# Optimization experiments

Hardware: AMD Instinct MI355X
Metric: run time of the kernel (lower is better)

The kernel has to match this reference:

```python
import jax, jax.numpy as jnp
import numpy as np

B, D, N, MSRC, H = 4, 256, 2048, 2048, 4
DIM = D // H  # per-head dim = 64
EPS = 1e-3


def _conv1x1(W, b, z):
    # 1x1 Conv1d == per-position linear: W [out,in], z [B,in,N]
    return jnp.einsum('oc,bcn->bon', W, z) + b[None, :, None]


def setup_inputs() -> dict:
    key = jax.random.key(0)
    ks = jax.random.split(key, 20)
    s = 0.05
    x = jax.random.normal(ks[0], (B, D, N), dtype=jnp.float32)
    source = jax.random.normal(ks[1], (B, D, MSRC), dtype=jnp.float32)
    mask = (jax.random.uniform(ks[2], (B, N, MSRC)) > 0.3).astype(jnp.float32)
    Wq = jax.random.normal(ks[3], (D, D), jnp.float32) * s
    bq = jax.random.normal(ks[4], (D,), jnp.float32) * s
    Wk = jax.random.normal(ks[5], (D, D), jnp.float32) * s
    bk = jax.random.normal(ks[6], (D,), jnp.float32) * s
    Wv = jax.random.normal(ks[7], (D, D), jnp.float32) * s
    bv = jax.random.normal(ks[8], (D,), jnp.float32) * s
    Wm = jax.random.normal(ks[9], (D, D), jnp.float32) * s
    bm = jax.random.normal(ks[10], (D,), jnp.float32) * s
    W1 = jax.random.normal(ks[11], (2 * D, 2 * D), jnp.float32) * s
    b1 = jax.random.normal(ks[12], (2 * D,), jnp.float32) * s
    gamma = jnp.ones((2 * D,), jnp.float32)
    beta = jnp.zeros((2 * D,), jnp.float32)
    rmean = jax.random.normal(ks[13], (2 * D,), jnp.float32) * 0.1
    rvar = jax.random.uniform(ks[14], (2 * D,), jnp.float32) + 0.5
    W2 = jax.random.normal(ks[15], (D, 2 * D), jnp.float32) * s
    b2 = jnp.zeros((D,), jnp.float32)  # nn.init.constant_(mlp[-1].bias, 0.0)
    return dict(x=x, source=source, mask=mask, Wq=Wq, bq=bq, Wk=Wk, bk=bk,
                Wv=Wv, bv=bv, Wm=Wm, bm=bm, W1=W1, b1=b1, gamma=gamma,
                beta=beta, rmean=rmean, rvar=rvar, W2=W2, b2=b2)


def reference(x, source, mask, Wq, bq, Wk, bk, Wv, bv, Wm, bm,
              W1, b1, gamma, beta, rmean, rvar, W2, b2):
    b = x.shape[0]
    # channel dim split as (dim, heads) per torch .view(B, dim, H, -1)
    q = _conv1x1(Wq, bq, x).reshape(b, DIM, H, -1)        # [B,d,H,N]
    k = _conv1x1(Wk, bk, source).reshape(b, DIM, H, -1)   # [B,d,H,M]
    v = _conv1x1(Wv, bv, source).reshape(b, DIM, H, -1)   # [B,d,H,M]
    scores = jnp.einsum('bdhn,bdhm->bhnm', q, k) / (DIM ** 0.5)
    neg = -jnp.finfo(scores.dtype).max
    scores = jnp.where(mask[:, None, :, :] > 0, scores, neg)
    prob = jax.nn.softmax(scores, axis=-1)                # [B,H,N,M]
    msg = jnp.einsum('bhnm,bdhm->bdhn', prob, v).reshape(b, D, -1)
    message = _conv1x1(Wm, bm, msg)                       # [B,D,N]
    y = jnp.concatenate([x, message], axis=1)             # [B,2D,N]
    h = _conv1x1(W1, b1, y)
    # BatchNorm1d (eval mode, eps=1e-3)
    h = (h - rmean[None, :, None]) * jax.lax.rsqrt(rvar + EPS)[None, :, None]
    h = h * gamma[None, :, None] + beta[None, :, None]
    h = jax.nn.relu(h)
    return _conv1x1(W2, b2, h)                            # [B,D,N]
```

## Files before the change

### kernel.cpp

```cpp
#include <hip/hip_runtime.h>

constexpr int Bb = 4;
constexpr int Dd = 256;
constexpr int Nn = 2048;
constexpr int Mm = 2048;
constexpr int Hh = 4;
constexpr int D2 = 512;
constexpr int NT = Bb * Nn;

#define FMAXV 3.402823466e38f

typedef _Float16 half8 __attribute__((ext_vector_type(8)));
typedef _Float16 half4v __attribute__((ext_vector_type(4)));
typedef float f32x4 __attribute__((ext_vector_type(4)));

typedef const __attribute__((address_space(1))) void* gas_p;
typedef __attribute__((address_space(3))) void* las_p;

__device__ __forceinline__ void gload16(const void* g, void* l) {
    __builtin_amdgcn_global_load_lds((gas_p)g, (las_p)l, 16, 0, 0);
}

__global__ __launch_bounds__(256)
void prep_all_kernel(const float* __restrict__ Wq, const float* __restrict__ bq,
                     const float* __restrict__ Wk, const float* __restrict__ bk,
                     const float* __restrict__ Wv, const float* __restrict__ bv,
                     const float* __restrict__ Wm,
                     const float* __restrict__ W1, const float* __restrict__ b1,
                     const float* __restrict__ gamma, const float* __restrict__ beta,
                     const float* __restrict__ rmean, const float* __restrict__ rvar,
                     const float* __restrict__ W2, const float* __restrict__ mask,
                     const float* __restrict__ x, const float* __restrict__ source,
                     _Float16* __restrict__ Wqp, float* __restrict__ bqp,
                     _Float16* __restrict__ Wkvp, float* __restrict__ bkvp,
                     _Float16* __restrict__ Wmp,
                     _Float16* __restrict__ W1p, float* __restrict__ b1f,
                     _Float16* __restrict__ W2p,
                     unsigned long long* __restrict__ bmask,
                     _Float16* __restrict__ Yp, _Float16* __restrict__ Sp) {
    const int r = blockIdx.x, t = threadIdx.x;
    if (r < 256) {
        const int h = r >> 6, d = r & 63, so = d * Hh + h;
        Wqp[r * 256 + t] = (_Float16)Wq[so * 256 + t];
        if (t == 0) bqp[r] = bq[so];
    } else if (r < 768) {
        const int rr = r - 256, part = rr >> 8, o = rr & 255;
        const int h = o >> 6, d = o & 63, so = d * Hh + h;
        const float* Ws = part ? Wv : Wk;
        const float* bs = part ? bv : bk;
        Wkvp[rr * 256 + t] = (_Float16)Ws[so * 256 + t];
        if (t == 0) bkvp[rr] = bs[so];
    } else if (r < 1024) {
        const int o = r - 768;
        const int h = t >> 6, d = t & 63, sk = d * Hh + h;
        Wmp[o * 256 + t] = (_Float16)Wm[o * 256 + sk];
    } else if (r < 1536) {
        const int o = r - 1024;
        const float s = gamma[o] * rsqrtf(rvar[o] + 1e-3f);
        W1p[o * 512 + t]       = (_Float16)(W1[o * 512 + t] * s);
        W1p[o * 512 + t + 256] = (_Float16)(W1[o * 512 + t + 256] * s);
        if (t == 0) b1f[o] = (b1[o] - rmean[o]) * s + beta[o];
    } else if (r < 1792) {
        const int o = r - 1536;
        W2p[o * 512 + t]       = (_Float16)W2[o * 512 + t];
        W2p[o * 512 + t + 256] = (_Float16)W2[o * 512 + t + 256];
    } else if (r < 3840) {
        const int id = r - 1792;
        const int w = t >> 6, lane = t & 63;
        const int row = id * 4 + w;
        const float* mrow = mask + (size_t)row * Mm;
        unsigned long long* brow = bmask + (size_t)row * (Mm / 64);
        #pragma unroll 4
        for (int word = 0; word < Mm / 64; ++word) {
            const float v = mrow[word * 64 + lane];
            const unsigned long long bits = __ballot(v > 0.f);
            if (lane == 0) brow[word] = bits;
        }
    } else {
        __shared__ _Float16 Ts[64][72];
        const int px = r - 3840;
        const int n0 = (px & 31) * 64, c0 = ((px >> 5) & 3) * 64;
        const int z = px >> 7, b = z >> 1, which = z & 1;
        const float* src = which ? source : x;
        _Float16* dst = which ? Sp : Yp;
        const int stride = which ? 256 : 512;
        const int cl = t >> 2, np = (t & 3) * 16;
        const float* sp = src + ((size_t)b * Dd + c0 + cl) * Nn + n0 + np;
        #pragma unroll
        for (int i = 0; i < 4; ++i) {
            float4 v = *(const float4*)(sp + i * 4);
            Ts[np + i * 4 + 0][cl] = (_Float16)v.x;
            Ts[np + i * 4 + 1][cl] = (_Float16)v.y;
            Ts[np + i * 4 + 2][cl] = (_Float16)v.z;
            Ts[np + i * 4 + 3][cl] = (_Float16)v.w;
        }
        __syncthreads();
        const int nl = t >> 2, cp = (t & 3) * 16;
        half8 a0 = *(const half8*)&Ts[nl][cp];
        half8 a1 = *(const half8*)&Ts[nl][cp + 8];
        _Float16* dp = dst + ((size_t)b * Nn + n0 + nl) * stride + c0 + cp;
        *(half8*)dp = a0;
        *(half8*)(dp + 8) = a1;
    }
}

__global__ __launch_bounds__(256)
void gemm4w_kernel(const _Float16* __restrict__ A, const _Float16* __restrict__ A2,
                   const _Float16* __restrict__ W, const float* __restrict__ bias,
                   _Float16* __restrict__ dst0, _Float16* __restrict__ dst1,
                   _Float16* __restrict__ dst2, float* __restrict__ dstF,
                   int K, int sA, int sOut, int modeSel, int relu, float oscale) {
    __shared__ __align__(16) _Float16 As[2 * 128 * 64];
    __shared__ __align__(16) _Float16 Bs[2 * 64 * 64];

    const int t = threadIdx.x;
    const int w = t >> 6, lane = t & 63, quad = lane >> 4, l16 = lane & 15;
    const int n0 = blockIdx.x * 128;
    const int og0 = blockIdx.y * 64;

    int mode = 0, oloc0 = og0;
    const _Float16* Ab = A;
    int sAl = sA;
    _Float16* d0 = dst0;
    float osc = oscale;
    if (modeSel == 3) {
        const int part = blockIdx.y >> 2;
        if (part == 1)      { Ab = A2; sAl = 256; d0 = dst1; oloc0 = og0 - 256; osc = 1.0f; }
        else if (part == 2) { Ab = A2; sAl = 256; mode = 1; oloc0 = og0 - 512; osc = 1.0f; }
    } else if (modeSel == 2) {
        mode = 2;
    }

    const int srow = t >> 3, sslot = t & 7;
    const int schunk = sslot ^ (srow & 7);

    f32x4 acc[2][4] = {};
    const int nk = K / 64;
    int buf = 0;

    {
        #pragma unroll
        for (int c = 0; c < 4; ++c)
            gload16(Ab + (size_t)(n0 + c * 32 + srow) * sAl + schunk * 8,
                    As + c * 2048 + t * 8);
        #pragma unroll
        for (int c = 0; c < 2; ++c)
            gload16(W + (size_t)(og0 + c * 32 + srow) * K + schunk * 8,
                    Bs + c * 2048 + t * 8);
        __asm__ volatile("s_waitcnt vmcnt(0)" ::: "memory");
        __syncthreads();
    }

    #pragma unroll 1
    for (int kt = 0; kt < nk; ++kt) {
        if (kt + 1 < nk) {
            const int k0 = (kt + 1) * 64, nb = buf ^ 1;
            #pragma unroll
            for (int c = 0; c < 4; ++c)
                gload16(Ab + (size_t)(n0 + c * 32 + srow) * sAl + k0 + schunk * 8,
                        As + nb * 8192 + c * 2048 + t * 8);
            #pragma unroll
            for (int c = 0; c < 2; ++c)
                gload16(W + (size_t)(og0 + c * 32 + srow) * K + k0 + schunk * 8,
                        Bs + nb * 4096 + c * 2048 + t * 8);
        }
        #pragma unroll
        for (int ks = 0; ks < 2; ++ks) {
            const int csw = ((ks * 4 + quad) ^ (l16 & 7)) * 8;
            half8 af[2], bf[4];
            #pragma unroll
            for (int i = 0; i < 2; ++i)
                af[i] = *(const half8*)&As[buf * 8192 + (w * 32 + i * 16 + l16) * 64 + csw];
            #pragma unroll
            for (int j = 0; j < 4; ++j)
                bf[j] = *(const half8*)&Bs[buf * 4096 + (j * 16 + l16) * 64 + csw];
            #pragma unroll
            for (int i = 0; i < 2; ++i)
                #pragma unroll
                for (int j = 0; j < 4; ++j)
                    acc[i][j] = __builtin_amdgcn_mfma_f32_16x16x32_f16(af[i], bf[j], acc[i][j], 0, 0, 0);
        }
        if (kt + 1 < nk) {
            __asm__ volatile("s_waitcnt vmcnt(0)" ::: "memory");
            __syncthreads();
            buf ^= 1;
        }
    }

    float bcol[4];
    #pragma unroll
    for (int j = 0; j < 4; ++j) bcol[j] = bias[og0 + j * 16 + l16];

    if (mode == 0) {
        _Float16* Escr = As + w * 2048;
        #pragma unroll
        for (int i = 0; i < 2; ++i) {
            #pragma unroll
            for (int j = 0; j < 4; ++j)
                #pragma unroll
                for (int reg = 0; reg < 4; ++reg) {
                    float v = (acc[i][j][reg] + bcol[j]) * osc;
                    if (relu) v = fmaxf(v, 0.f);
                    Escr[(quad * 4 + reg) * 72 + j * 16 + l16] = (_Float16)v;
                }
            __asm__ volatile("s_waitcnt lgkmcnt(0)" ::: "memory");
            const int row = lane & 15, oseg = (lane >> 4) * 16;
            half8 e0 = *(const half8*)&Escr[row * 72 + oseg];
            half8 e1 = *(const half8*)&Escr[row * 72 + oseg + 8];
            _Float16* dp = d0 + (size_t)(n0 + w * 32 + i * 16 + row) * sOut + oloc0 + oseg;
            *(half8*)dp = e0;
            *(half8*)(dp + 8) = e1;
            __asm__ volatile("s_waitcnt lgkmcnt(0)" ::: "memory");
        }
    } else if (mode == 1) {
        #pragma unroll
        for (int i = 0; i < 2; ++i)
            #pragma unroll
            for (int j = 0; j < 4; ++j) {
                const int c = j * 16 + l16;
                const int mloc = w * 32 + i * 16 + quad * 4;
                const int sw = l16 * 8;
                half4v pv;
                #pragma unroll
                for (int reg = 0; reg < 4; ++reg)
                    pv[reg] = (_Float16)(acc[i][j][reg] + bcol[j]);
                *(half4v*)&As[c * 128 + (mloc ^ sw)] = pv;
            }
        __syncthreads();
        const int n0m = n0 & 2047, bidx = n0 >> 11;
        #pragma unroll
        for (int r = 0; r < 2; ++r) {
            const int c = (t >> 3) + r * 32;
            const int mch = (t & 7) * 16;
            const int sw = (c & 15) * 8;
            half8 v0 = *(const half8*)&As[c * 128 + (mch ^ sw)];
            half8 v1 = *(const half8*)&As[c * 128 + ((mch + 8) ^ sw)];
            _Float16* dp = dst2 + ((size_t)bidx * 256 + oloc0 + c) * (size_t)Mm + n0m + mch;
            *(half8*)dp = v0;
            *(half8*)(dp + 8) = v1;
        }
    } else {
        __syncthreads();
        float* scr = (float*)As;
        #pragma unroll
        for (int i = 0; i < 2; ++i)
            #pragma unroll
            for (int j = 0; j < 4; ++j) {
                const int c = j * 16 + l16;
                const int mloc = w * 32 + i * 16 + quad * 4;
                const int sw = (c & 7) * 4;
                f32x4 v;
                #pragma unroll
                for (int reg = 0; reg < 4; ++reg) v[reg] = acc[i][j][reg] + bcol[j];
                *(f32x4*)&scr[c * 128 + (mloc ^ sw)] = v;
            }
        __syncthreads();
        const int n0m = n0 & 2047, bidx = n0 >> 11;
        #pragma unroll
        for (int r = 0; r < 2; ++r) {
            const int c = (t >> 3) + r * 32;
            const int mch = (t & 7) * 16;
            const int sw = (c & 7) * 4;
            float* dp = dstF + ((size_t)bidx * 256 + og0 + c) * (size_t)Nn + n0m + mch;
            #pragma unroll
            for (int k = 0; k < 4; ++k)
                *(f32x4*)(dp + k * 4) = *(const f32x4*)&scr[c * 128 + ((mch + k * 4) ^ sw)];
        }
    }
}

__global__ __launch_bounds__(256)
void attn_mfma_kernel(const _Float16* __restrict__ Qp, const _Float16* __restrict__ Kp,
                      const _Float16* __restrict__ Vt,
                      const unsigned int* __restrict__ bmask,
                      _Float16* __restrict__ Oa, _Float16* __restrict__ Ob,
                      float* __restrict__ La, float* __restrict__ Lb) {
    __shared__ __align__(16) _Float16 Ks[64][72];
    __shared__ __align__(16) _Float16 Vs[64][72];
    __shared__ __align__(16) _Float16 Ps[4][16][72];

    const int id = blockIdx.x;
    const int xcd = id & 7, loc = id >> 3;
    const int bh = xcd * 2 + (loc >> 6);
    const int sub = loc & 63;
    const int mhalf = sub & 1;
    const int n0 = (sub >> 1) * 64;
    const int b = bh >> 2, h = bh & 3;

    const int t = threadIdx.x;
    const int w = t >> 6, lane = t & 63, quad = lane >> 4, l16 = lane & 15;

    const _Float16* qp = Qp + ((size_t)b * Nn + n0 + w * 16 + l16) * 256 + h * 64 + quad * 8;
    const half8 qa0 = *(const half8*)(qp);
    const half8 qa1 = *(const half8*)(qp + 32);

    const _Float16* Kstg = Kp + (size_t)b * Nn * 256 + h * 64;
    const _Float16* Vstg = Vt + ((size_t)b * 256 + h * 64) * (size_t)Mm;
    const int sr = t >> 2, sc = (t & 3) * 16;

    const unsigned int* bmBase = bmask + ((size_t)b * Nn + n0 + w * 16 + quad * 4) * (Mm / 32);

    _Float16* Od = mhalf ? Ob : Oa;
    float* Ld = mhalf ? Lb : La;
    const int mbeg = mhalf * (Mm / 2);

    float lo[4] = {0.f, 0.f, 0.f, 0.f};
    f32x4 O[4] = {};

    half8 sk0, sk1, sv0, sv1;
    auto stage_load = [&](int m0) {
        const _Float16* ks = Kstg + (size_t)(m0 + sr) * 256 + sc;
        sk0 = *(const half8*)(ks);
        sk1 = *(const half8*)(ks + 8);
        const _Float16* vs = Vstg + (size_t)sr * Mm + m0 + sc;
        sv0 = *(const half8*)(vs);
        sv1 = *(const half8*)(vs + 8);
    };
    auto stage_write = [&]() {
        *(half8*)&Ks[sr][sc]     = sk0;
        *(half8*)&Ks[sr][sc + 8] = sk1;
        *(half8*)&Vs[sr][sc]     = sv0;
        *(half8*)&Vs[sr][sc + 8] = sv1;
    };

    stage_load(mbeg);
    stage_write();
    __syncthreads();

    #pragma unroll 1
    for (int it = 0; it < (Mm / 2) / 64; ++it) {
        const int m0 = mbeg + it * 64;
        if (it < (Mm / 2) / 64 - 1) stage_load(m0 + 64);

        uint2 bmv[4];
        #pragma unroll
        for (int reg = 0; reg < 4; ++reg)
            bmv[reg] = *(const uint2*)(bmBase + (size_t)reg * (Mm / 32) + (m0 >> 5));

        f32x4 S[4];
        #pragma unroll
        for (int mt = 0; mt < 4; ++mt) {
            half8 k0 = *(const half8*)&Ks[mt * 16 + l16][quad * 8];
            half8 k1 = *(const half8*)&Ks[mt * 16 + l16][32 + quad * 8];
            f32x4 z = {0.f, 0.f, 0.f, 0.f};
            z = __builtin_amdgcn_mfma_f32_16x16x32_f16(qa0, k0, z, 0, 0, 0);
            z = __builtin_amdgcn_mfma_f32_16x16x32_f16(qa1, k1, z, 0, 0, 0);
            S[mt] = z;
        }

        float p[4][4];
        #pragma unroll
        for (int reg = 0; reg < 4; ++reg) {
            const unsigned losh = bmv[reg].x >> l16;
            const unsigned hish = bmv[reg].y >> l16;
            p[0][reg] = (losh & 1u)         ? __expf(S[0][reg]) : 0.f;
            p[1][reg] = ((losh >> 16) & 1u) ? __expf(S[1][reg]) : 0.f;
            p[2][reg] = (hish & 1u)         ? __expf(S[2][reg]) : 0.f;
            p[3][reg] = ((hish >> 16) & 1u) ? __expf(S[3][reg]) : 0.f;
        }
        #pragma unroll
        for (int reg = 0; reg < 4; ++reg)
            lo[reg] += (p[0][reg] + p[1][reg]) + (p[2][reg] + p[3][reg]);

        #pragma unroll
        for (int mt = 0; mt < 4; ++mt)
            #pragma unroll
            for (int reg = 0; reg < 4; ++reg)
                Ps[w][quad * 4 + reg][mt * 16 + l16] = (_Float16)p[mt][reg];
        __asm__ volatile("s_waitcnt lgkmcnt(0)" ::: "memory");
        half8 pa0 = *(const half8*)&Ps[w][l16][quad * 8];
        half8 pa1 = *(const half8*)&Ps[w][l16][32 + quad * 8];

        #pragma unroll
        for (int dt = 0; dt < 4; ++dt) {
            half8 v0 = *(const half8*)&Vs[dt * 16 + l16][quad * 8];
            half8 v1 = *(const half8*)&Vs[dt * 16 + l16][32 + quad * 8];
            O[dt] = __builtin_amdgcn_mfma_f32_16x16x32_f16(pa0, v0, O[dt], 0, 0, 0);
            O[dt] = __builtin_amdgcn_mfma_f32_16x16x32_f16(pa1, v1, O[dt], 0, 0, 0);
        }

        if (it < (Mm / 2) / 64 - 1) {
            __syncthreads();
            stage_write();
            __syncthreads();
        }
    }

    #pragma unroll
    for (int reg = 0; reg < 4; ++reg) {
        float s = lo[reg];
        s += __shfl_xor(s, 1);
        s += __shfl_xor(s, 2);
        s += __shfl_xor(s, 4);
        s += __shfl_xor(s, 8);
        lo[reg] = s;
    }

    _Float16* op = Od + ((size_t)b * Nn + n0 + w * 16 + quad * 4) * 256 + h * 64 + l16;
    #pragma unroll
    for (int reg = 0; reg < 4; ++reg)
        #pragma unroll
        for (int dt = 0; dt < 4; ++dt)
            op[(size_t)reg * 256 + dt * 16] = (_Float16)(O[dt][reg] * 0.0625f);
    if (l16 == 0) {
        #pragma unroll
        for (int reg = 0; reg < 4; ++reg)
            Ld[((size_t)b * Nn + n0 + w * 16 + quad * 4 + reg) * 4 + h] = lo[reg] * 0.0625f;
    }
}

__global__ __launch_bounds__(256)
void gemm_msg_kernel(const _Float16* __restrict__ Oa, const _Float16* __restrict__ Ob,
                     const float* __restrict__ La, const float* __restrict__ Lb,
                     const _Float16* __restrict__ W, const float* __restrict__ bias,
                     _Float16* __restrict__ dst) {
    __shared__ __align__(16) _Float16 As[2 * 128 * 64];
    __shared__ __align__(16) _Float16 Bs[2 * 64 * 64];

    const int t = threadIdx.x;
    const int w = t >> 6, lane = t & 63, quad = lane >> 4, l16 = lane & 15;
    const int n0 = blockIdx.x * 128;
    const int og0 = blockIdx.y * 64;
    const int srow = t >> 3, sslot = t & 7;
    const int schunk = sslot ^ (srow & 7);
    constexpr int K = 256;

    f32x4 acc[2][4] = {};

    half8 oa[4], ob[4];
    float inv[4];

    auto loadA = [&](int k0) {
        const int h = k0 >> 6;
        #pragma unroll
        for (int c = 0; c < 4; ++c) {
            const size_t row = (size_t)(n0 + c * 32 + srow);
            oa[c] = *(const half8*)(Oa + row * 256 + k0 + schunk * 8);
            ob[c] = *(const half8*)(Ob + row * 256 + k0 + schunk * 8);
            inv[c] = 1.0f / (La[row * 4 + h] + Lb[row * 4 + h]);
        }
    };
    auto writeA = [&](int nb) {
        #pragma unroll
        for (int c = 0; c < 4; ++c) {
            half8 m;
            #pragma unroll
            for (int k = 0; k < 8; ++k)
                m[k] = (_Float16)(((float)oa[c][k] + (float)ob[c][k]) * inv[c]);
            *(half8*)&As[nb * 8192 + c * 2048 + t * 8] = m;
        }
    };
    auto loadB = [&](int k0, int nb) {
        #pragma unroll
        for (int c = 0; c < 2; ++c)
            gload16(W + (size_t)(og0 + c * 32 + srow) * K + k0 + schunk * 8,
                    Bs + nb * 4096 + c * 2048 + t * 8);
    };

    loadA(0);
    loadB(0, 0);
    writeA(0);
    __asm__ volatile("s_waitcnt vmcnt(0)" ::: "memory");
    __syncthreads();

    int buf = 0;
    #pragma unroll 1
    for (int kt = 0; kt < 4; ++kt) {
        if (kt < 3) {
            loadA((kt + 1) * 64);
            loadB((kt + 1) * 64, buf ^ 1);
        }
        #pragma unroll
        for (int ks = 0; ks < 2; ++ks) {
            const int csw = ((ks * 4 + quad) ^ (l16 & 7)) * 8;
            half8 af[2], bf[4];
            #pragma unroll
            for (int i = 0; i < 2; ++i)
                af[i] = *(const half8*)&As[buf * 8192 + (w * 32 + i * 16 + l16) * 64 + csw];
            #pragma unroll
            for (int j = 0; j < 4; ++j)
                bf[j] = *(const half8*)&Bs[buf * 4096 + (j * 16 + l16) * 64 + csw];
            #pragma unroll
            for (int i = 0; i < 2; ++i)
                #pragma unroll
                for (int j = 0; j < 4; ++j)
                    acc[i][j] = __builtin_amdgcn_mfma_f32_16x16x32_f16(af[i], bf[j], acc[i][j], 0, 0, 0);
        }
        if (kt < 3) {
            writeA(buf ^ 1);
            __asm__ volatile("s_waitcnt vmcnt(0)" ::: "memory");
            __syncthreads();
            buf ^= 1;
        }
    }

    float bcol[4];
    #pragma unroll
    for (int j = 0; j < 4; ++j) bcol[j] = bias[og0 + j * 16 + l16];

    _Float16* Escr = As + w * 2048;
    #pragma unroll
    for (int i = 0; i < 2; ++i) {
        #pragma unroll
        for (int j = 0; j < 4; ++j)
            #pragma unroll
            for (int reg = 0; reg < 4; ++reg)
                Escr[(quad * 4 + reg) * 72 + j * 16 + l16] =
                    (_Float16)(acc[i][j][reg] + bcol[j]);
        __asm__ volatile("s_waitcnt lgkmcnt(0)" ::: "memory");
        const int row = lane & 15, oseg = (lane >> 4) * 16;
        half8 e0 = *(const half8*)&Escr[row * 72 + oseg];
        half8 e1 = *(const half8*)&Escr[row * 72 + oseg + 8];
        _Float16* dp = dst + (size_t)(n0 + w * 32 + i * 16 + row) * 512 + og0 + oseg;
        *(half8*)dp = e0;
        *(half8*)(dp + 8) = e1;
        __asm__ volatile("s_waitcnt lgkmcnt(0)" ::: "memory");
    }
}

extern "C" void kernel_launch(void* const* d_in, const int* in_sizes, int n_in,
                              void* d_out, int out_size, void* d_ws, size_t ws_size,
                              hipStream_t stream) {
    const float* x      = (const float*)d_in[0];
    const float* source = (const float*)d_in[1];
    const float* mask   = (const float*)d_in[2];
    const float* Wq = (const float*)d_in[3];
    const float* bq = (const float*)d_in[4];
    const float* Wk = (const float*)d_in[5];
    const float* bk = (const float*)d_in[6];
    const float* Wv = (const float*)d_in[7];
    const float* bv = (const float*)d_in[8];
    const float* Wm = (const float*)d_in[9];
    const float* bm = (const float*)d_in[10];
    const float* W1 = (const float*)d_in[11];
    const float* b1 = (const float*)d_in[12];
    const float* gamma = (const float*)d_in[13];
    const float* beta  = (const float*)d_in[14];
    const float* rmean = (const float*)d_in[15];
    const float* rvar  = (const float*)d_in[16];
    const float* W2 = (const float*)d_in[17];
    const float* b2 = (const float*)d_in[18];
    float* outp = (float*)d_out;

    char* wsb = (char*)d_ws;
    _Float16* Yp   = (_Float16*)wsb;
    _Float16* Sp   = (_Float16*)(wsb + (8u << 20));
    _Float16* Qp   = (_Float16*)(wsb + (12u << 20));
    _Float16* Kp   = (_Float16*)(wsb + (16u << 20));
    _Float16* Vt   = (_Float16*)(wsb + (20u << 20));
    _Float16* Oa   = (_Float16*)(wsb + (24u << 20));
    _Float16* Hp   = (_Float16*)(wsb + (28u << 20));
    unsigned long long* bmask = (unsigned long long*)(wsb + (28u << 20));
    _Float16* Ob = (_Float16*)(wsb + (30u << 20));
    float* La = (float*)(wsb + (34u << 20));
    float* Lb = (float*)(wsb + (34u << 20) + (128u << 10));
    char* wp = wsb + (36u << 20);
    _Float16* Wqp  = (_Float16*)wp;            wp += 256 * 256 * 2;
    _Float16* Wkvp = (_Float16*)wp;            wp += 512 * 256 * 2;
    _Float16* Wmp  = (_Float16*)wp;            wp += 256 * 256 * 2;
    _Float16* W1p  = (_Float16*)wp;            wp += 512 * 512 * 2;
    _Float16* W2p  = (_Float16*)wp;            wp += 256 * 512 * 2;
    float* bqp  = (float*)wp;                  wp += 256 * 4;
    float* bkvp = (float*)wp;                  wp += 512 * 4;
    float* b1f  = (float*)wp;                  wp += 512 * 4;

    prep_all_kernel<<<4864, 256, 0, stream>>>(
        Wq, bq, Wk, bk, Wv, bv, Wm, W1, b1, gamma, beta, rmean, rvar, W2, mask,
        x, source, Wqp, bqp, Wkvp, bkvp, Wmp, W1p, b1f, W2p, bmask, Yp, Sp);

    gemm4w_kernel<<<dim3(NT / 128, 12), 256, 0, stream>>>(
        Yp, Sp, Wqp, bqp, Qp, Kp, Vt, nullptr, 256, 512, 256, 3, 0, 0.125f);

    attn_mfma_kernel<<<1024, 256, 0, stream>>>(Qp, Kp, Vt,
                                               (const unsigned int*)bmask,
                                               Oa, Ob, La, Lb);

    gemm_msg_kernel<<<dim3(NT / 128, 4), 256, 0, stream>>>(
        Oa, Ob, La, Lb, Wmp, bm, Yp + 256);

    gemm4w_kernel<<<dim3(NT / 128, 8), 256, 0, stream>>>(
        Yp, nullptr, W1p, b1f, Hp, nullptr, nullptr, nullptr, 512, 512, 512, 0, 1, 1.0f);
    gemm4w_kernel<<<dim3(NT / 128, 4), 256, 0, stream>>>(
        Hp, nullptr, W2p, b2, nullptr, nullptr, nullptr, outp, 512, 512, 0, 2, 0, 1.0f);
}
```

Before: 233.3 us.

## Split attention KV range into four partitions and XOR-swizzle K/V LDS tiles

The attention kernel now splits the key range into four quarters instead of two, doubling the grid to 2048 blocks. Each block writes partial outputs and row sums to one of four buffers, and the message GEMM merges all four. The Sp buffer and the final output buffer are reused as scratch for the extra partials. K/V shared tiles drop their padding and use an XOR swizzle on 16-byte chunks to avoid bank conflicts. The change adds more partial-result traffic and merge work, and depends on the reused buffers being dead at this point.

```diff
diff --git a/kernel.cpp b/kernel.cpp
--- a/kernel.cpp
+++ b/kernel.cpp
@@ -274,17 +274,19 @@
                       const _Float16* __restrict__ Vt,
                       const unsigned int* __restrict__ bmask,
                       _Float16* __restrict__ Oa, _Float16* __restrict__ Ob,
-                      float* __restrict__ La, float* __restrict__ Lb) {
-    __shared__ __align__(16) _Float16 Ks[64][72];
-    __shared__ __align__(16) _Float16 Vs[64][72];
+                      _Float16* __restrict__ Oc, _Float16* __restrict__ Od,
+                      float* __restrict__ La, float* __restrict__ Lb,
+                      float* __restrict__ Lc, float* __restrict__ Ld) {
+    __shared__ __align__(16) _Float16 Ks[64][64];
+    __shared__ __align__(16) _Float16 Vs[64][64];
     __shared__ __align__(16) _Float16 Ps[4][16][72];
 
     const int id = blockIdx.x;
     const int xcd = id & 7, loc = id >> 3;
-    const int bh = xcd * 2 + (loc >> 6);
-    const int sub = loc & 63;
-    const int mhalf = sub & 1;
-    const int n0 = (sub >> 1) * 64;
+    const int bh = xcd * 2 + (loc >> 7);
+    const int sub = loc & 127;
+    const int mquart = sub & 3;
+    const int n0 = (sub >> 2) * 64;
     const int b = bh >> 2, h = bh & 3;
 
     const int t = threadIdx.x;
@@ -296,13 +298,16 @@
 
     const _Float16* Kstg = Kp + (size_t)b * Nn * 256 + h * 64;
     const _Float16* Vstg = Vt + ((size_t)b * 256 + h * 64) * (size_t)Mm;
-    const int sr = t >> 2, sc = (t & 3) * 16;
+    const int sr = t >> 2;
+    const int sc = (t & 3) * 16;
+    const int ss0 = ((t & 3) * 2) ^ (sr & 7);
+    const int ss1 = ((t & 3) * 2 + 1) ^ (sr & 7);
 
     const unsigned int* bmBase = bmask + ((size_t)b * Nn + n0 + w * 16 + quad * 4) * (Mm / 32);
 
-    _Float16* Od = mhalf ? Ob : Oa;
-    float* Ld = mhalf ? Lb : La;
-    const int mbeg = mhalf * (Mm / 2);
+    _Float16* Odst = mquart == 0 ? Oa : mquart == 1 ? Ob : mquart == 2 ? Oc : Od;
+    float*    Ldst = mquart == 0 ? La : mquart == 1 ? Lb : mquart == 2 ? Lc : Ld;
+    const int mbeg = mquart * (Mm / 4);
 
     float lo[4] = {0.f, 0.f, 0.f, 0.f};
     f32x4 O[4] = {};
@@ -317,10 +322,10 @@
         sv1 = *(const half8*)(vs + 8);
     };
     auto stage_write = [&]() {
-        *(half8*)&Ks[sr][sc]     = sk0;
-        *(half8*)&Ks[sr][sc + 8] = sk1;
-        *(half8*)&Vs[sr][sc]     = sv0;
-        *(half8*)&Vs[sr][sc + 8] = sv1;
+        *(half8*)&Ks[sr][ss0 * 8] = sk0;
+        *(half8*)&Ks[sr][ss1 * 8] = sk1;
+        *(half8*)&Vs[sr][ss0 * 8] = sv0;
+        *(half8*)&Vs[sr][ss1 * 8] = sv1;
     };
 
     stage_load(mbeg);
@@ -328,9 +333,9 @@
     __syncthreads();
 
     #pragma unroll 1
-    for (int it = 0; it < (Mm / 2) / 64; ++it) {
+    for (int it = 0; it < (Mm / 4) / 64; ++it) {
         const int m0 = mbeg + it * 64;
-        if (it < (Mm / 2) / 64 - 1) stage_load(m0 + 64);
+        if (it < (Mm / 4) / 64 - 1) stage_load(m0 + 64);
 
         uint2 bmv[4];
         #pragma unroll
@@ -340,8 +345,9 @@
         f32x4 S[4];
         #pragma unroll
         for (int mt = 0; mt < 4; ++mt) {
-            half8 k0 = *(const half8*)&Ks[mt * 16 + l16][quad * 8];
-            half8 k1 = *(const half8*)&Ks[mt * 16 + l16][32 + quad * 8];
+            const int r = mt * 16 + l16, rs = r & 7;
+            half8 k0 = *(const half8*)&Ks[r][(quad ^ rs) * 8];
+            half8 k1 = *(const half8*)&Ks[r][((quad + 4) ^ rs) * 8];
             f32x4 z = {0.f, 0.f, 0.f, 0.f};
             z = __builtin_amdgcn_mfma_f32_16x16x32_f16(qa0, k0, z, 0, 0, 0);
             z = __builtin_amdgcn_mfma_f32_16x16x32_f16(qa1, k1, z, 0, 0, 0);
@@ -373,13 +379,14 @@
 
         #pragma unroll
         for (int dt = 0; dt < 4; ++dt) {
-            half8 v0 = *(const half8*)&Vs[dt * 16 + l16][quad * 8];
-            half8 v1 = *(const half8*)&Vs[dt * 16 + l16][32 + quad * 8];
+            const int r = dt * 16 + l16, rs = r & 7;
+            half8 v0 = *(const half8*)&Vs[r][(quad ^ rs) * 8];
+            half8 v1 = *(const half8*)&Vs[r][((quad + 4) ^ rs) * 8];
             O[dt] = __builtin_amdgcn_mfma_f32_16x16x32_f16(pa0, v0, O[dt], 0, 0, 0);
             O[dt] = __builtin_amdgcn_mfma_f32_16x16x32_f16(pa1, v1, O[dt], 0, 0, 0);
         }
 
-        if (it < (Mm / 2) / 64 - 1) {
+        if (it < (Mm / 4) / 64 - 1) {
             __syncthreads();
             stage_write();
             __syncthreads();
@@ -396,7 +403,7 @@
         lo[reg] = s;
     }
 
-    _Float16* op = Od + ((size_t)b * Nn + n0 + w * 16 + quad * 4) * 256 + h * 64 + l16;
+    _Float16* op = Odst + ((size_t)b * Nn + n0 + w * 16 + quad * 4) * 256 + h * 64 + l16;
     #pragma unroll
     for (int reg = 0; reg < 4; ++reg)
         #pragma unroll
@@ -405,13 +412,15 @@
     if (l16 == 0) {
         #pragma unroll
         for (int reg = 0; reg < 4; ++reg)
-            Ld[((size_t)b * Nn + n0 + w * 16 + quad * 4 + reg) * 4 + h] = lo[reg] * 0.0625f;
+            Ldst[((size_t)b * Nn + n0 + w * 16 + quad * 4 + reg) * 4 + h] = lo[reg] * 0.0625f;
     }
 }
 
 __global__ __launch_bounds__(256)
 void gemm_msg_kernel(const _Float16* __restrict__ Oa, const _Float16* __restrict__ Ob,
+                     const _Float16* __restrict__ Oc, const _Float16* __restrict__ Od,
                      const float* __restrict__ La, const float* __restrict__ Lb,
+                     const float* __restrict__ Lc, const float* __restrict__ Ld,
                      const _Float16* __restrict__ W, const float* __restrict__ bias,
                      _Float16* __restrict__ dst) {
     __shared__ __align__(16) _Float16 As[2 * 128 * 64];
@@ -427,7 +436,7 @@
 
     f32x4 acc[2][4] = {};
 
-    half8 oa[4], ob[4];
+    half8 oa[4], ob[4], oc[4], od[4];
     float inv[4];
 
     auto loadA = [&](int k0) {
@@ -435,9 +444,13 @@
         #pragma unroll
         for (int c = 0; c < 4; ++c) {
             const size_t row = (size_t)(n0 + c * 32 + srow);
-            oa[c] = *(const half8*)(Oa + row * 256 + k0 + schunk * 8);
-            ob[c] = *(const half8*)(Ob + row * 256 + k0 + schunk * 8);
-            inv[c] = 1.0f / (La[row * 4 + h] + Lb[row * 4 + h]);
+            const size_t off = row * 256 + k0 + schunk * 8;
+            oa[c] = *(const half8*)(Oa + off);
+            ob[c] = *(const half8*)(Ob + off);
+            oc[c] = *(const half8*)(Oc + off);
+            od[c] = *(const half8*)(Od + off);
+            inv[c] = 1.0f / (La[row * 4 + h] + Lb[row * 4 + h]
+                           + Lc[row * 4 + h] + Ld[row * 4 + h]);
         }
     };
     auto writeA = [&](int nb) {
@@ -446,7 +459,8 @@
             half8 m;
             #pragma unroll
             for (int k = 0; k < 8; ++k)
-                m[k] = (_Float16)(((float)oa[c][k] + (float)ob[c][k]) * inv[c]);
+                m[k] = (_Float16)((((float)oa[c][k] + (float)ob[c][k])
+                                 + ((float)oc[c][k] + (float)od[c][k])) * inv[c]);
             *(half8*)&As[nb * 8192 + c * 2048 + t * 8] = m;
         }
     };
@@ -554,6 +568,10 @@
     _Float16* Ob = (_Float16*)(wsb + (30u << 20));
     float* La = (float*)(wsb + (34u << 20));
     float* Lb = (float*)(wsb + (34u << 20) + (128u << 10));
+    float* Lc = (float*)(wsb + (34u << 20) + (256u << 10));
+    float* Ld = (float*)(wsb + (34u << 20) + (384u << 10));
+    _Float16* Oc = Sp;
+    _Float16* Od = (_Float16*)outp;
     char* wp = wsb + (36u << 20);
     _Float16* Wqp  = (_Float16*)wp;            wp += 256 * 256 * 2;
     _Float16* Wkvp = (_Float16*)wp;            wp += 512 * 256 * 2;
@@ -571,12 +589,12 @@
     gemm4w_kernel<<<dim3(NT / 128, 12), 256, 0, stream>>>(
         Yp, Sp, Wqp, bqp, Qp, Kp, Vt, nullptr, 256, 512, 256, 3, 0, 0.125f);
 
-    attn_mfma_kernel<<<1024, 256, 0, stream>>>(Qp, Kp, Vt,
+    attn_mfma_kernel<<<2048, 256, 0, stream>>>(Qp, Kp, Vt,
                                                (const unsigned int*)bmask,
-                                               Oa, Ob, La, Lb);
+                                               Oa, Ob, Oc, Od, La, Lb, Lc, Ld);
 
     gemm_msg_kernel<<<dim3(NT / 128, 4), 256, 0, stream>>>(
-        Oa, Ob, La, Lb, Wmp, bm, Yp + 256);
+        Oa, Ob, Oc, Od, La, Lb, Lc, Ld, Wmp, bm, Yp + 256);
 
     gemm4w_kernel<<<dim3(NT / 128, 8), 256, 0, stream>>>(
         Yp, nullptr, W1p, b1f, Hp, nullptr, nullptr, nullptr, 512, 512, 512, 0, 1, 1.0f);
```

After: 239.7 us. 2.7% more time.

## Swap QK MFMA operands, swizzle K/V LDS, use exp2 with folded log2e

Applied to the files above, without the earlier changes.

The QK^T MFMA now takes K as the A operand, so each lane holds scores for one query row across four keys. This lets the mask come from a single uint2 load per row, lets the row sum live in one scalar reduced with two shuffles, and lets P be written to LDS as packed half4 stores. The K/V LDS tiles drop their padding in favour of an XOR swizzle, and exp is replaced by exp2 with log2(e) folded into the Q projection scale. The changes cut LDS traffic, mask loads and conversion work, but depend on the swizzle and operand-swap indexing being exactly right.

```diff
diff --git a/kernel.cpp b/kernel.cpp
--- a/kernel.cpp
+++ b/kernel.cpp
@@ -12,6 +12,7 @@
 
 typedef _Float16 half8 __attribute__((ext_vector_type(8)));
 typedef _Float16 half4v __attribute__((ext_vector_type(4)));
+typedef _Float16 half2v __attribute__((ext_vector_type(2)));
 typedef float f32x4 __attribute__((ext_vector_type(4)));
 
 typedef const __attribute__((address_space(1))) void* gas_p;
@@ -275,8 +276,8 @@
                       const unsigned int* __restrict__ bmask,
                       _Float16* __restrict__ Oa, _Float16* __restrict__ Ob,
                       float* __restrict__ La, float* __restrict__ Lb) {
-    __shared__ __align__(16) _Float16 Ks[64][72];
-    __shared__ __align__(16) _Float16 Vs[64][72];
+    __shared__ __align__(16) _Float16 Ks[64][64];
+    __shared__ __align__(16) _Float16 Vs[64][64];
     __shared__ __align__(16) _Float16 Ps[4][16][72];
 
     const int id = blockIdx.x;
@@ -296,15 +297,18 @@
 
     const _Float16* Kstg = Kp + (size_t)b * Nn * 256 + h * 64;
     const _Float16* Vstg = Vt + ((size_t)b * 256 + h * 64) * (size_t)Mm;
-    const int sr = t >> 2, sc = (t & 3) * 16;
-
-    const unsigned int* bmBase = bmask + ((size_t)b * Nn + n0 + w * 16 + quad * 4) * (Mm / 32);
-
-    _Float16* Od = mhalf ? Ob : Oa;
-    float* Ld = mhalf ? Lb : La;
+    const int sr = t >> 2;
+    const int sc = (t & 3) * 16;
+    const int ss0 = ((t & 3) * 2) ^ (sr & 7);
+    const int ss1 = ((t & 3) * 2 + 1) ^ (sr & 7);
+
+    const unsigned int* bmRow = bmask + ((size_t)b * Nn + n0 + w * 16 + l16) * (Mm / 32);
+
+    _Float16* Odst = mhalf ? Ob : Oa;
+    float*    Ldst = mhalf ? Lb : La;
     const int mbeg = mhalf * (Mm / 2);
 
-    float lo[4] = {0.f, 0.f, 0.f, 0.f};
+    float psum = 0.f;
     f32x4 O[4] = {};
 
     half8 sk0, sk1, sv0, sv1;
@@ -317,10 +321,10 @@
         sv1 = *(const half8*)(vs + 8);
     };
     auto stage_write = [&]() {
-        *(half8*)&Ks[sr][sc]     = sk0;
-        *(half8*)&Ks[sr][sc + 8] = sk1;
-        *(half8*)&Vs[sr][sc]     = sv0;
-        *(half8*)&Vs[sr][sc + 8] = sv1;
+        *(half8*)&Ks[sr][ss0 * 8] = sk0;
+        *(half8*)&Ks[sr][ss1 * 8] = sk1;
+        *(half8*)&Vs[sr][ss0 * 8] = sv0;
+        *(half8*)&Vs[sr][ss1 * 8] = sv1;
     };
 
     stage_load(mbeg);
@@ -332,49 +336,46 @@
         const int m0 = mbeg + it * 64;
         if (it < (Mm / 2) / 64 - 1) stage_load(m0 + 64);
 
-        uint2 bmv[4];
-        #pragma unroll
-        for (int reg = 0; reg < 4; ++reg)
-            bmv[reg] = *(const uint2*)(bmBase + (size_t)reg * (Mm / 32) + (m0 >> 5));
+        const uint2 bmv = *(const uint2*)(bmRow + (m0 >> 5));
 
         f32x4 S[4];
         #pragma unroll
         for (int mt = 0; mt < 4; ++mt) {
-            half8 k0 = *(const half8*)&Ks[mt * 16 + l16][quad * 8];
-            half8 k1 = *(const half8*)&Ks[mt * 16 + l16][32 + quad * 8];
+            const int r = mt * 16 + l16, rs = r & 7;
+            half8 k0 = *(const half8*)&Ks[r][(quad ^ rs) * 8];
+            half8 k1 = *(const half8*)&Ks[r][((quad + 4) ^ rs) * 8];
             f32x4 z = {0.f, 0.f, 0.f, 0.f};
-            z = __builtin_amdgcn_mfma_f32_16x16x32_f16(qa0, k0, z, 0, 0, 0);
-            z = __builtin_amdgcn_mfma_f32_16x16x32_f16(qa1, k1, z, 0, 0, 0);
+            z = __builtin_amdgcn_mfma_f32_16x16x32_f16(k0, qa0, z, 0, 0, 0);
+            z = __builtin_amdgcn_mfma_f32_16x16x32_f16(k1, qa1, z, 0, 0, 0);
             S[mt] = z;
         }
 
-        float p[4][4];
-        #pragma unroll
-        for (int reg = 0; reg < 4; ++reg) {
-            const unsigned losh = bmv[reg].x >> l16;
-            const unsigned hish = bmv[reg].y >> l16;
-            p[0][reg] = (losh & 1u)         ? __expf(S[0][reg]) : 0.f;
-            p[1][reg] = ((losh >> 16) & 1u) ? __expf(S[1][reg]) : 0.f;
-            p[2][reg] = (hish & 1u)         ? __expf(S[2][reg]) : 0.f;
-            p[3][reg] = ((hish >> 16) & 1u) ? __expf(S[3][reg]) : 0.f;
-        }
-        #pragma unroll
-        for (int reg = 0; reg < 4; ++reg)
-            lo[reg] += (p[0][reg] + p[1][reg]) + (p[2][reg] + p[3][reg]);
-
-        #pragma unroll
-        for (int mt = 0; mt < 4; ++mt)
-            #pragma unroll
-            for (int reg = 0; reg < 4; ++reg)
-                Ps[w][quad * 4 + reg][mt * 16 + l16] = (_Float16)p[mt][reg];
+        const unsigned losh = bmv.x >> (quad * 4);
+        const unsigned hish = bmv.y >> (quad * 4);
+        #pragma unroll
+        for (int mt = 0; mt < 4; ++mt) {
+            const unsigned wb = (mt < 2) ? losh : hish;
+            const int sh = (mt & 1) * 16;
+            const float p0 = ((wb >> (sh + 0)) & 1u) ? __builtin_exp2f(S[mt][0]) : 0.f;
+            const float p1 = ((wb >> (sh + 1)) & 1u) ? __builtin_exp2f(S[mt][1]) : 0.f;
+            const float p2 = ((wb >> (sh + 2)) & 1u) ? __builtin_exp2f(S[mt][2]) : 0.f;
+            const float p3 = ((wb >> (sh + 3)) & 1u) ? __builtin_exp2f(S[mt][3]) : 0.f;
+            psum += (p0 + p1) + (p2 + p3);
+            const half2v lo2 = __builtin_bit_cast(half2v, __builtin_amdgcn_cvt_pkrtz(p0, p1));
+            const half2v hi2 = __builtin_bit_cast(half2v, __builtin_amdgcn_cvt_pkrtz(p2, p3));
+            half4v pv;
+            pv[0] = lo2[0]; pv[1] = lo2[1]; pv[2] = hi2[0]; pv[3] = hi2[1];
+            *(half4v*)&Ps[w][l16][mt * 16 + quad * 4] = pv;
+        }
         __asm__ volatile("s_waitcnt lgkmcnt(0)" ::: "memory");
         half8 pa0 = *(const half8*)&Ps[w][l16][quad * 8];
         half8 pa1 = *(const half8*)&Ps[w][l16][32 + quad * 8];
 
         #pragma unroll
         for (int dt = 0; dt < 4; ++dt) {
-            half8 v0 = *(const half8*)&Vs[dt * 16 + l16][quad * 8];
-            half8 v1 = *(const half8*)&Vs[dt * 16 + l16][32 + quad * 8];
+            const int r = dt * 16 + l16, rs = r & 7;
+            half8 v0 = *(const half8*)&Vs[r][(quad ^ rs) * 8];
+            half8 v1 = *(const half8*)&Vs[r][((quad + 4) ^ rs) * 8];
             O[dt] = __builtin_amdgcn_mfma_f32_16x16x32_f16(pa0, v0, O[dt], 0, 0, 0);
             O[dt] = __builtin_amdgcn_mfma_f32_16x16x32_f16(pa1, v1, O[dt], 0, 0, 0);
         }
@@ -386,27 +387,17 @@
         }
     }
 
-    #pragma unroll
-    for (int reg = 0; reg < 4; ++reg) {
-        float s = lo[reg];
-        s += __shfl_xor(s, 1);
-        s += __shfl_xor(s, 2);
-        s += __shfl_xor(s, 4);
-        s += __shfl_xor(s, 8);
-        lo[reg] = s;
-    }
-
-    _Float16* op = Od + ((size_t)b * Nn + n0 + w * 16 + quad * 4) * 256 + h * 64 + l16;
+    psum += __shfl_xor(psum, 16);
+    psum += __shfl_xor(psum, 32);
+
+    _Float16* op = Odst + ((size_t)b * Nn + n0 + w * 16 + quad * 4) * 256 + h * 64 + l16;
     #pragma unroll
     for (int reg = 0; reg < 4; ++reg)
         #pragma unroll
         for (int dt = 0; dt < 4; ++dt)
             op[(size_t)reg * 256 + dt * 16] = (_Float16)(O[dt][reg] * 0.0625f);
-    if (l16 == 0) {
-        #pragma unroll
-        for (int reg = 0; reg < 4; ++reg)
-            Ld[((size_t)b * Nn + n0 + w * 16 + quad * 4 + reg) * 4 + h] = lo[reg] * 0.0625f;
-    }
+    if (lane < 16)
+        Ldst[((size_t)b * Nn + n0 + w * 16 + l16) * 4 + h] = psum * 0.0625f;
 }
 
 __global__ __launch_bounds__(256)
@@ -435,8 +426,9 @@
         #pragma unroll
         for (int c = 0; c < 4; ++c) {
             const size_t row = (size_t)(n0 + c * 32 + srow);
-            oa[c] = *(const half8*)(Oa + row * 256 + k0 + schunk * 8);
-            ob[c] = *(const half8*)(Ob + row * 256 + k0 + schunk * 8);
+            const size_t off = row * 256 + k0 + schunk * 8;
+            oa[c] = *(const half8*)(Oa + off);
+            ob[c] = *(const half8*)(Ob + off);
             inv[c] = 1.0f / (La[row * 4 + h] + Lb[row * 4 + h]);
         }
     };
@@ -569,7 +561,7 @@
         x, source, Wqp, bqp, Wkvp, bkvp, Wmp, W1p, b1f, W2p, bmask, Yp, Sp);
 
     gemm4w_kernel<<<dim3(NT / 128, 12), 256, 0, stream>>>(
-        Yp, Sp, Wqp, bqp, Qp, Kp, Vt, nullptr, 256, 512, 256, 3, 0, 0.125f);
+        Yp, Sp, Wqp, bqp, Qp, Kp, Vt, nullptr, 256, 512, 256, 3, 0, 0.18033688011f);
 
     attn_mfma_kernel<<<1024, 256, 0, stream>>>(Qp, Kp, Vt,
                                                (const unsigned int*)bmask,
```

Result: slower. 239.3 us (+2.6%).
